# Performance work log

Measured on AMD Instinct MI355X. Metric: run time of the kernel, lower is better.

The kernel has to match this reference:

```python
import jax, jax.numpy as jnp
import numpy as np

NUM_EMBEDDINGS = 512
EMBEDDING_DIM = 64
COMMITMENT_COST = 0.25
DECAY = 0.99
EPSILON = 1e-05


def setup_inputs() -> dict:
    key = jax.random.key(0)
    k1, k2, k3 = jax.random.split(key, 3)
    inputs = jax.random.normal(k1, (32, 64, 64, EMBEDDING_DIM), dtype=jnp.float32)
    emb_w = jax.random.normal(k2, (NUM_EMBEDDINGS, EMBEDDING_DIM), dtype=jnp.float32)
    ema_cluster_size = jnp.ones((NUM_EMBEDDINGS,), dtype=jnp.float32)
    ema_w = jax.random.normal(k3, (NUM_EMBEDDINGS, EMBEDDING_DIM), dtype=jnp.float32)
    return {"inputs": inputs, "emb_w": emb_w,
            "ema_cluster_size": ema_cluster_size, "ema_w": ema_w}


def reference(inputs, emb_w, ema_cluster_size, ema_w):
    """VQ-VAE EMA quantizer forward (training=True path).

    inputs:           [B, H, W, D]  NHWC latents
    emb_w:            [K, D]        codebook (pre-update)
    ema_cluster_size: [K]           EMA cluster-size buffer
    ema_w:            [K, D]        EMA weight buffer
    """
    B, H, W, D = inputs.shape
    K = emb_w.shape[0]
    flat = inputs.reshape(-1, D)                                  # [N, D]

    distances = (jnp.sum(flat * flat, axis=1, keepdims=True)
                 - 2.0 * flat @ emb_w.T
                 + jnp.sum(emb_w * emb_w, axis=1))
    encoding_indices = jnp.argmin(distances, axis=1)              # [N]
    encodings = jax.nn.one_hot(encoding_indices, K, dtype=flat.dtype)  # [N, K]

    # --- EMA codebook update (buffer math; no gradient flows here) ---
    counts = jax.lax.stop_gradient(jnp.sum(encodings, axis=0))    # [K]
    cs = ema_cluster_size * DECAY + (1.0 - DECAY) * counts
    n = jnp.sum(cs)
    cs = (cs + EPSILON) / (n + K * EPSILON) * n                   # Laplace smoothing
    dw = jax.ops.segment_sum(jax.lax.stop_gradient(flat),
                             encoding_indices, num_segments=K)    # [K, D]
    new_ema_w = ema_w * DECAY + (1.0 - DECAY) * dw
    new_emb = new_ema_w / cs[:, None]                             # updated codebook

    # Quantize with the updated codebook (gather)
    quantized = new_emb[encoding_indices].reshape(B, H, W, D)

    # Commitment loss (quantized is detached)
    e_latent_loss = jnp.mean((jax.lax.stop_gradient(quantized) - inputs) ** 2)
    loss = COMMITMENT_COST * e_latent_loss

    # Straight-through estimator
    quantized_st = inputs + jax.lax.stop_gradient(quantized - inputs)

    avg_probs = jnp.mean(encodings, axis=0)
    perplexity = jnp.exp(-jnp.sum(avg_probs * jnp.log(avg_probs + 1e-10)))

    # NHWC -> NCHW as in the original return
    return loss, jnp.transpose(quantized_st, (0, 3, 1, 2)), perplexity, encodings
```

## Files before the change

kernel.cpp:

```cpp
#include <hip/hip_runtime.h>

#define DIM 64
#define K_CODES 512
#define N_VEC 131072
#define CREP 16
#define DREP 64
#define Q_OFF 1
#define PERP_OFF 8388609
#define ENC_OFF 8388610

using bfrag = __attribute__((ext_vector_type(8))) short;
using ffrag = __attribute__((ext_vector_type(4))) float;

__device__ __forceinline__ void split3(float x, short& h0, short& h1, short& h2)
{
    unsigned u0 = __float_as_uint(x);
    h0 = (short)(u0 >> 16);
    float r = x - __uint_as_float(u0 & 0xFFFF0000u);
    unsigned u1 = __float_as_uint(r);
    h1 = (short)(u1 >> 16);
    float r2 = r - __uint_as_float(u1 & 0xFFFF0000u);
    h2 = (short)(__float_as_uint(r2) >> 16);
}

__global__ __launch_bounds__(256) void epack_ee_kernel(
    const float* __restrict__ emb_w,
    bfrag* __restrict__ epack,
    float* __restrict__ ee,
    float* __restrict__ crep,
    float* __restrict__ lossac)
{
    __shared__ float part[2][16][8];
    const int tl = threadIdx.x;
    const int t = blockIdx.x * 256 + tl;
    const int lane = t & 63;
    const int db = (t >> 6) & 1;
    const int ctl = tl >> 7;
    const int ct = t >> 7;
    const int r16 = lane & 15, quad = lane >> 4;
    const int c  = ct * 16 + r16;
    const int d0 = db * 32 + quad * 8;
    const float* src = emb_w + (size_t)c * DIM + d0;

    crep[t] = 0.f;
    crep[4096 + t] = 0.f;
    if (t == 0) lossac[0] = 0.f;

    bfrag f0, f1, f2;
    float ssum = 0.f;
#pragma unroll
    for (int j = 0; j < 8; ++j) {
        const float x = src[j];
        ssum = fmaf(x, x, ssum);
        short a, b, cc;
        split3(x, a, b, cc);
        f0[j] = a; f1[j] = b; f2[j] = cc;
    }
    const int base = (ct * 2 + db) * 3;
    epack[(base + 0) * 64 + lane] = f0;
    epack[(base + 1) * 64 + lane] = f1;
    epack[(base + 2) * 64 + lane] = f2;

    part[ctl][r16][db * 4 + quad] = ssum;
    __syncthreads();
    if (tl < 32) {
        const int cl = tl >> 4, r = tl & 15;
        float s = 0.f;
#pragma unroll
        for (int i = 0; i < 8; ++i) s += part[cl][r][i];
        ee[(blockIdx.x * 2 + cl) * 16 + r] = s;
    }
}

__global__ __launch_bounds__(256, 4) void argmin_mfma_kernel(
    const float* __restrict__ inputs,
    const bfrag* __restrict__ epack,
    const float* __restrict__ eeg,
    int* __restrict__ idx,
    float* __restrict__ counts_rep)
{
    const int t = threadIdx.x;
    const int lane = t & 63;
    const int r16 = lane & 15;
    const int quad = lane >> 4;
    const size_t v0 = (size_t)blockIdx.x * 128 + (t >> 6) * 32;

    bfrag xf[2][2][3];
#pragma unroll
    for (int rt = 0; rt < 2; ++rt)
#pragma unroll
        for (int db = 0; db < 2; ++db) {
            const float* src = inputs + (v0 + rt * 16 + r16) * DIM + db * 32 + quad * 8;
            const float4 va = *reinterpret_cast<const float4*>(src);
            const float4 vb = *reinterpret_cast<const float4*>(src + 4);
            float vals[8] = {va.x, va.y, va.z, va.w, vb.x, vb.y, vb.z, vb.w};
            bfrag f0, f1, f2;
#pragma unroll
            for (int j = 0; j < 8; ++j) {
                short a, b, c;
                split3(vals[j], a, b, c);
                f0[j] = a; f1[j] = b; f2[j] = c;
            }
            xf[rt][db][0] = f0; xf[rt][db][1] = f1; xf[rt][db][2] = f2;
        }

    float best[2][4];
    int bestk[2][4];
#pragma unroll
    for (int a = 0; a < 2; ++a)
#pragma unroll
        for (int b = 0; b < 4; ++b) { best[a][b] = 3.4e38f; bestk[a][b] = 0; }

    constexpr int PI[6] = {0, 0, 1, 0, 2, 1};
    constexpr int PJ[6] = {0, 1, 0, 2, 0, 1};

    for (int ct = 0; ct < 32; ++ct) {
        bfrag e[2][3];
#pragma unroll
        for (int db = 0; db < 2; ++db)
#pragma unroll
            for (int s = 0; s < 3; ++s)
                e[db][s] = epack[((ct * 2 + db) * 3 + s) * 64 + lane];
        const float eel = eeg[ct * 16 + r16];

        ffrag acc[2];
        acc[0] = (ffrag){0.f, 0.f, 0.f, 0.f};
        acc[1] = (ffrag){0.f, 0.f, 0.f, 0.f};
#pragma unroll
        for (int db = 0; db < 2; ++db)
#pragma unroll
            for (int p = 0; p < 6; ++p) {
                acc[0] = __builtin_amdgcn_mfma_f32_16x16x32_bf16(
                    xf[0][db][PI[p]], e[db][PJ[p]], acc[0], 0, 0, 0);
                acc[1] = __builtin_amdgcn_mfma_f32_16x16x32_bf16(
                    xf[1][db][PI[p]], e[db][PJ[p]], acc[1], 0, 0, 0);
            }

        const int kc = ct * 16 + r16;
#pragma unroll
        for (int rt = 0; rt < 2; ++rt)
#pragma unroll
            for (int rg = 0; rg < 4; ++rg) {
                const float dist = fmaf(-2.f, acc[rt][rg], eel);
                if (dist < best[rt][rg]) { best[rt][rg] = dist; bestk[rt][rg] = kc; }
            }
    }

#pragma unroll
    for (int rt = 0; rt < 2; ++rt)
#pragma unroll
        for (int rg = 0; rg < 4; ++rg) {
            float b = best[rt][rg];
            int k = bestk[rt][rg];
#pragma unroll
            for (int m = 1; m < 16; m <<= 1) {
                const float ob = __shfl_xor(b, m, 64);
                const int ok = __shfl_xor(k, m, 64);
                if (ob < b || (ob == b && ok < k)) { b = ob; k = ok; }
            }
            bestk[rt][rg] = k;
        }

    if (r16 == 0) {
        float* crep = counts_rep + (blockIdx.x & (CREP - 1)) * K_CODES;
#pragma unroll
        for (int rt = 0; rt < 2; ++rt)
#pragma unroll
            for (int rg = 0; rg < 4; ++rg) {
                const int v = rt * 16 + quad * 4 + rg;
                const int k = bestk[rt][rg];
                idx[v0 + v] = k;
                atomicAdd(&crep[k], 1.0f);
            }
    }
}

__global__ __launch_bounds__(256) void enc_write_kernel(
    const int* __restrict__ idx,
    float* __restrict__ enc,
    float* __restrict__ dwrep)
{
    const size_t nf4 = 16777215;
    float4* body = reinterpret_cast<float4*>(enc + 2);
    const size_t stride = (size_t)gridDim.x * 256;

    for (size_t g = (size_t)blockIdx.x * 256 + threadIdx.x; g < nf4; g += stride) {
        const size_t e0 = 4 * g + 2;
        const int r0 = (int)(e0 >> 9);
        const int r1 = (int)((e0 + 3) >> 9);
        const int i0 = idx[r0];
        const int i1 = (r1 != r0) ? idx[r1] : i0;
        float4 v;
        v.x = ((int)(e0 & 511) == i0) ? 1.f : 0.f;
        v.y = ((int)((e0 + 1) & 511) == (((e0 + 1) >> 9) == (size_t)r0 ? i0 : i1)) ? 1.f : 0.f;
        v.z = ((int)((e0 + 2) & 511) == (((e0 + 2) >> 9) == (size_t)r0 ? i0 : i1)) ? 1.f : 0.f;
        v.w = ((int)((e0 + 3) & 511) == (((e0 + 3) >> 9) == (size_t)r0 ? i0 : i1)) ? 1.f : 0.f;
        body[g] = v;
    }

    float4* dw4 = reinterpret_cast<float4*>(dwrep);
    const size_t ndw4 = (size_t)DREP * K_CODES * DIM / 4;
    const float4 z = make_float4(0.f, 0.f, 0.f, 0.f);
    for (size_t i = (size_t)blockIdx.x * 256 + threadIdx.x; i < ndw4; i += stride)
        dw4[i] = z;

    if (blockIdx.x == 0 && threadIdx.x == 0) {
        const int k0 = idx[0];
        enc[0] = (k0 == 0) ? 1.f : 0.f;
        enc[1] = (k0 == 1) ? 1.f : 0.f;
        const int kL = idx[N_VEC - 1];
        enc[67108862] = (kL == 510) ? 1.f : 0.f;
        enc[67108863] = (kL == 511) ? 1.f : 0.f;
    }
}

__global__ __launch_bounds__(256) void dw_scatter_kernel(
    const float* __restrict__ inputs,
    const int* __restrict__ idx,
    float* __restrict__ dwrep)
{
    __shared__ int sIdx[256];
    const int t = threadIdx.x;
    const size_t vbase = (size_t)blockIdx.x * 256;
    sIdx[t] = idx[vbase + t];
    __syncthreads();
    const int w = t >> 6, lane = t & 63;
    const int v0 = w * 64;
#pragma unroll 4
    for (int j = 0; j < 64; ++j) {
        const int v = v0 + j;
        const int k = sIdx[v];
        const float xv = inputs[(vbase + v) * DIM + lane];
        atomicAdd(&dwrep[((size_t)(v & (DREP - 1)) << 15) + (k << 6) + lane], xv);
    }
}

__global__ __launch_bounds__(512) void emaA_kernel(
    const float* __restrict__ counts_rep,
    const float* __restrict__ ema_cs,
    float* __restrict__ csbuf,
    float* __restrict__ perp_out)
{
    __shared__ float red[K_CODES];
    const int k = threadIdx.x;
    float cnt = 0.f;
#pragma unroll
    for (int r = 0; r < CREP; ++r) cnt += counts_rep[r * K_CODES + k];
    float cs = ema_cs[k] * 0.99f + 0.01f * cnt;

    red[k] = cs;
    __syncthreads();
    for (int s = K_CODES / 2; s > 0; s >>= 1) {
        if (k < s) red[k] += red[k + s];
        __syncthreads();
    }
    const float n = red[0];
    __syncthreads();

    csbuf[k] = (cs + 1e-5f) / (n + (float)K_CODES * 1e-5f) * n;

    const float p = cnt * (1.0f / (float)N_VEC);
    red[k] = p * logf(p + 1e-10f);
    __syncthreads();
    for (int s = K_CODES / 2; s > 0; s >>= 1) {
        if (k < s) red[k] += red[k + s];
        __syncthreads();
    }
    if (k == 0) perp_out[0] = expf(-red[0]);
}

__global__ __launch_bounds__(256) void emaB_kernel(
    const float* __restrict__ dwrep,
    const float* __restrict__ ema_w,
    const float* __restrict__ csbuf,
    float* __restrict__ new_emb)
{
    const int t = blockIdx.x * 256 + threadIdx.x;
    const int k = t >> 6;
    float dwv = 0.f;
#pragma unroll
    for (int r = 0; r < DREP; ++r) dwv += dwrep[((size_t)r << 15) + t];
    const float v = ema_w[t] * 0.99f + 0.01f * dwv;
    new_emb[t] = v / csbuf[k];
}

__global__ __launch_bounds__(256) void quantize_kernel(
    const float* __restrict__ inputs,
    const int* __restrict__ idx,
    const float* __restrict__ new_emb,
    float* __restrict__ out_q,
    float* __restrict__ loss_accum)
{
    __shared__ int sIdx[64];
    __shared__ float tile[DIM][65];
    __shared__ float wsum[4];

    const int bh = blockIdx.x;
    const int b = bh >> 6, h = bh & 63;
    const int t = threadIdx.x;

    if (t < 64) sIdx[t] = idx[bh * 64 + t];
    __syncthreads();

    const float* inRow = inputs + (size_t)bh * 64 * DIM;
    const int d = t & 63;
    const int wg = t >> 6;
    float lsum = 0.f;
#pragma unroll
    for (int p = 0; p < 16; ++p) {
        const int w = wg * 16 + p;
        const float xv = inRow[w * DIM + d];
        const float qv = new_emb[sIdx[w] * DIM + d];
        const float diff = qv - xv;
        tile[d][w] = xv + diff;
        lsum = fmaf(diff, diff, lsum);
    }
    __syncthreads();

    const int w2 = t & 63;
    const int dg = t >> 6;
#pragma unroll
    for (int p = 0; p < 16; ++p) {
        const int d2 = dg * 16 + p;
        out_q[(((size_t)b * DIM + d2) * 64 + h) * 64 + w2] = tile[d2][w2];
    }

    for (int off = 32; off > 0; off >>= 1) lsum += __shfl_down(lsum, off);
    if ((t & 63) == 0) wsum[t >> 6] = lsum;
    __syncthreads();
    if (t == 0) atomicAdd(loss_accum, (wsum[0] + wsum[1]) + (wsum[2] + wsum[3]));
}

__global__ void finalize_kernel(const float* __restrict__ loss_accum,
                                float* __restrict__ out_loss)
{
    out_loss[0] = 0.25f * (loss_accum[0] / 8388608.0f);
}

extern "C" void kernel_launch(void* const* d_in, const int* in_sizes, int n_in,
                              void* d_out, int out_size, void* d_ws, size_t ws_size,
                              hipStream_t stream)
{
    const float* inputs = (const float*)d_in[0];
    const float* emb_w  = (const float*)d_in[1];
    const float* ema_cs = (const float*)d_in[2];
    const float* ema_w  = (const float*)d_in[3];
    float* out = (float*)d_out;
    float* ws  = (float*)d_ws;

    int*   idxbuf  = (int*)ws;
    float* crep    = ws + 131072;
    float* lossac  = ws + 139264;
    float* csbuf   = ws + 139265;
    float* eebuf   = ws + 139777;
    float* nemb    = ws + 140289;
    bfrag* epack   = (bfrag*)(ws + 173060);

    float* dwrep = out + 16;

    epack_ee_kernel<<<16, 256, 0, stream>>>(emb_w, epack, eebuf, crep, lossac);

    argmin_mfma_kernel<<<N_VEC / 128, 256, 0, stream>>>(
        inputs, epack, eebuf, idxbuf, crep);

    enc_write_kernel<<<2048, 256, 0, stream>>>(idxbuf, out + ENC_OFF, dwrep);

    dw_scatter_kernel<<<N_VEC / 256, 256, 0, stream>>>(inputs, idxbuf, dwrep);

    emaA_kernel<<<1, K_CODES, 0, stream>>>(crep, ema_cs, csbuf, out + PERP_OFF);
    emaB_kernel<<<K_CODES * DIM / 256, 256, 0, stream>>>(dwrep, ema_w, csbuf, nemb);

    quantize_kernel<<<32 * 64, 256, 0, stream>>>(
        inputs, idxbuf, nemb, out + Q_OFF, lossac);

    finalize_kernel<<<1, 1, 0, stream>>>(lossac, out);
}
```

Before: 216.7 us.

## Widen argmin tiles, fold dw zeroing into argmin, merge scatter with one-hot write

The argmin kernel now handles 256 vectors per block (four row tiles per wave instead of two), so each codebook fragment loaded is reused across more MFMAs. To fit the extra registers, launch bounds drop from 4 to 2 blocks per CU. The zeroing of the replicated dw buffer moves into the argmin kernel, each block clearing 1024 float4s. The dw scatter and one-hot encoding write are merged into a single launch with block-range dispatch, so the atomic scatter overlaps the bandwidth-bound encoding store and one launch is removed. The cost is lower occupancy in argmin and fewer grid-stride blocks writing the encodings.

```diff
diff --git a/kernel.cpp b/kernel.cpp
--- a/kernel.cpp
+++ b/kernel.cpp
@@ -8,6 +8,9 @@
 #define Q_OFF 1
 #define PERP_OFF 8388609
 #define ENC_OFF 8388610
+
+#define DW_BLOCKS 512
+#define ENC_BLOCKS 1280
 
 using bfrag = __attribute__((ext_vector_type(8))) short;
 using ffrag = __attribute__((ext_vector_type(4))) float;
@@ -72,22 +75,30 @@
     }
 }
 
-__global__ __launch_bounds__(256, 4) void argmin_mfma_kernel(
+__global__ __launch_bounds__(256, 2) void argmin_mfma_kernel(
     const float* __restrict__ inputs,
     const bfrag* __restrict__ epack,
     const float* __restrict__ eeg,
     int* __restrict__ idx,
-    float* __restrict__ counts_rep)
+    float* __restrict__ counts_rep,
+    float* __restrict__ dwrep)
 {
     const int t = threadIdx.x;
     const int lane = t & 63;
     const int r16 = lane & 15;
     const int quad = lane >> 4;
-    const size_t v0 = (size_t)blockIdx.x * 128 + (t >> 6) * 32;
-
-    bfrag xf[2][2][3];
-#pragma unroll
-    for (int rt = 0; rt < 2; ++rt)
+    const size_t v0 = (size_t)blockIdx.x * 256 + (t >> 6) * 64;
+
+    {
+        float4* z4 = reinterpret_cast<float4*>(dwrep) + (size_t)blockIdx.x * 1024;
+        const float4 z = make_float4(0.f, 0.f, 0.f, 0.f);
+#pragma unroll
+        for (int i = 0; i < 4; ++i) z4[i * 256 + t] = z;
+    }
+
+    bfrag xf[4][2][3];
+#pragma unroll
+    for (int rt = 0; rt < 4; ++rt)
 #pragma unroll
         for (int db = 0; db < 2; ++db) {
             const float* src = inputs + (v0 + rt * 16 + r16) * DIM + db * 32 + quad * 8;
@@ -104,16 +115,17 @@
             xf[rt][db][0] = f0; xf[rt][db][1] = f1; xf[rt][db][2] = f2;
         }
 
-    float best[2][4];
-    int bestk[2][4];
-#pragma unroll
-    for (int a = 0; a < 2; ++a)
+    float best[4][4];
+    int bestk[4][4];
+#pragma unroll
+    for (int a = 0; a < 4; ++a)
 #pragma unroll
         for (int b = 0; b < 4; ++b) { best[a][b] = 3.4e38f; bestk[a][b] = 0; }
 
     constexpr int PI[6] = {0, 0, 1, 0, 2, 1};
     constexpr int PJ[6] = {0, 1, 0, 2, 0, 1};
 
+#pragma unroll 2
     for (int ct = 0; ct < 32; ++ct) {
         bfrag e[2][3];
 #pragma unroll
@@ -123,22 +135,22 @@
                 e[db][s] = epack[((ct * 2 + db) * 3 + s) * 64 + lane];
         const float eel = eeg[ct * 16 + r16];
 
-        ffrag acc[2];
-        acc[0] = (ffrag){0.f, 0.f, 0.f, 0.f};
-        acc[1] = (ffrag){0.f, 0.f, 0.f, 0.f};
+        ffrag acc[4];
+#pragma unroll
+        for (int rt = 0; rt < 4; ++rt) acc[rt] = (ffrag){0.f, 0.f, 0.f, 0.f};
+
 #pragma unroll
         for (int db = 0; db < 2; ++db)
 #pragma unroll
-            for (int p = 0; p < 6; ++p) {
-                acc[0] = __builtin_amdgcn_mfma_f32_16x16x32_bf16(
-                    xf[0][db][PI[p]], e[db][PJ[p]], acc[0], 0, 0, 0);
-                acc[1] = __builtin_amdgcn_mfma_f32_16x16x32_bf16(
-                    xf[1][db][PI[p]], e[db][PJ[p]], acc[1], 0, 0, 0);
-            }
+            for (int p = 0; p < 6; ++p)
+#pragma unroll
+                for (int rt = 0; rt < 4; ++rt)
+                    acc[rt] = __builtin_amdgcn_mfma_f32_16x16x32_bf16(
+                        xf[rt][db][PI[p]], e[db][PJ[p]], acc[rt], 0, 0, 0);
 
         const int kc = ct * 16 + r16;
 #pragma unroll
-        for (int rt = 0; rt < 2; ++rt)
+        for (int rt = 0; rt < 4; ++rt)
 #pragma unroll
             for (int rg = 0; rg < 4; ++rg) {
                 const float dist = fmaf(-2.f, acc[rt][rg], eel);
@@ -147,7 +159,7 @@
     }
 
 #pragma unroll
-    for (int rt = 0; rt < 2; ++rt)
+    for (int rt = 0; rt < 4; ++rt)
 #pragma unroll
         for (int rg = 0; rg < 4; ++rg) {
             float b = best[rt][rg];
@@ -164,7 +176,7 @@
     if (r16 == 0) {
         float* crep = counts_rep + (blockIdx.x & (CREP - 1)) * K_CODES;
 #pragma unroll
-        for (int rt = 0; rt < 2; ++rt)
+        for (int rt = 0; rt < 4; ++rt)
 #pragma unroll
             for (int rg = 0; rg < 4; ++rg) {
                 const int v = rt * 16 + quad * 4 + rg;
@@ -175,63 +187,57 @@
     }
 }
 
-__global__ __launch_bounds__(256) void enc_write_kernel(
+__global__ __launch_bounds__(256) void encdw_kernel(
+    const float* __restrict__ inputs,
     const int* __restrict__ idx,
     float* __restrict__ enc,
     float* __restrict__ dwrep)
 {
-    const size_t nf4 = 16777215;
-    float4* body = reinterpret_cast<float4*>(enc + 2);
-    const size_t stride = (size_t)gridDim.x * 256;
-
-    for (size_t g = (size_t)blockIdx.x * 256 + threadIdx.x; g < nf4; g += stride) {
-        const size_t e0 = 4 * g + 2;
-        const int r0 = (int)(e0 >> 9);
-        const int r1 = (int)((e0 + 3) >> 9);
-        const int i0 = idx[r0];
-        const int i1 = (r1 != r0) ? idx[r1] : i0;
-        float4 v;
-        v.x = ((int)(e0 & 511) == i0) ? 1.f : 0.f;
-        v.y = ((int)((e0 + 1) & 511) == (((e0 + 1) >> 9) == (size_t)r0 ? i0 : i1)) ? 1.f : 0.f;
-        v.z = ((int)((e0 + 2) & 511) == (((e0 + 2) >> 9) == (size_t)r0 ? i0 : i1)) ? 1.f : 0.f;
-        v.w = ((int)((e0 + 3) & 511) == (((e0 + 3) >> 9) == (size_t)r0 ? i0 : i1)) ? 1.f : 0.f;
-        body[g] = v;
-    }
-
-    float4* dw4 = reinterpret_cast<float4*>(dwrep);
-    const size_t ndw4 = (size_t)DREP * K_CODES * DIM / 4;
-    const float4 z = make_float4(0.f, 0.f, 0.f, 0.f);
-    for (size_t i = (size_t)blockIdx.x * 256 + threadIdx.x; i < ndw4; i += stride)
-        dw4[i] = z;
-
-    if (blockIdx.x == 0 && threadIdx.x == 0) {
-        const int k0 = idx[0];
-        enc[0] = (k0 == 0) ? 1.f : 0.f;
-        enc[1] = (k0 == 1) ? 1.f : 0.f;
-        const int kL = idx[N_VEC - 1];
-        enc[67108862] = (kL == 510) ? 1.f : 0.f;
-        enc[67108863] = (kL == 511) ? 1.f : 0.f;
-    }
-}
-
-__global__ __launch_bounds__(256) void dw_scatter_kernel(
-    const float* __restrict__ inputs,
-    const int* __restrict__ idx,
-    float* __restrict__ dwrep)
-{
-    __shared__ int sIdx[256];
+    const int bid = blockIdx.x;
     const int t = threadIdx.x;
-    const size_t vbase = (size_t)blockIdx.x * 256;
-    sIdx[t] = idx[vbase + t];
-    __syncthreads();
-    const int w = t >> 6, lane = t & 63;
-    const int v0 = w * 64;
+
+    if (bid < DW_BLOCKS) {
+        __shared__ int sIdx[256];
+        const size_t vbase = (size_t)bid * 256;
+        sIdx[t] = idx[vbase + t];
+        __syncthreads();
+        const int w = t >> 6, lane = t & 63;
+        const int v0 = w * 64;
 #pragma unroll 4
-    for (int j = 0; j < 64; ++j) {
-        const int v = v0 + j;
-        const int k = sIdx[v];
-        const float xv = inputs[(vbase + v) * DIM + lane];
-        atomicAdd(&dwrep[((size_t)(v & (DREP - 1)) << 15) + (k << 6) + lane], xv);
+        for (int j = 0; j < 64; ++j) {
+            const int v = v0 + j;
+            const int k = sIdx[v];
+            const float xv = inputs[(vbase + v) * DIM + lane];
+            atomicAdd(&dwrep[((size_t)(v & (DREP - 1)) << 15) + (k << 6) + lane], xv);
+        }
+    } else {
+        const int eb = bid - DW_BLOCKS;
+        const size_t nf4 = 16777215;
+        float4* body = reinterpret_cast<float4*>(enc + 2);
+        const size_t stride = (size_t)ENC_BLOCKS * 256;
+
+        for (size_t g = (size_t)eb * 256 + t; g < nf4; g += stride) {
+            const size_t e0 = 4 * g + 2;
+            const int r0 = (int)(e0 >> 9);
+            const int r1 = (int)((e0 + 3) >> 9);
+            const int i0 = idx[r0];
+            const int i1 = (r1 != r0) ? idx[r1] : i0;
+            float4 v;
+            v.x = ((int)(e0 & 511) == i0) ? 1.f : 0.f;
+            v.y = ((int)((e0 + 1) & 511) == (((e0 + 1) >> 9) == (size_t)r0 ? i0 : i1)) ? 1.f : 0.f;
+            v.z = ((int)((e0 + 2) & 511) == (((e0 + 2) >> 9) == (size_t)r0 ? i0 : i1)) ? 1.f : 0.f;
+            v.w = ((int)((e0 + 3) & 511) == (((e0 + 3) >> 9) == (size_t)r0 ? i0 : i1)) ? 1.f : 0.f;
+            body[g] = v;
+        }
+
+        if (eb == 0 && t == 0) {
+            const int k0 = idx[0];
+            enc[0] = (k0 == 0) ? 1.f : 0.f;
+            enc[1] = (k0 == 1) ? 1.f : 0.f;
+            const int kL = idx[N_VEC - 1];
+            enc[67108862] = (kL == 510) ? 1.f : 0.f;
+            enc[67108863] = (kL == 511) ? 1.f : 0.f;
+        }
     }
 }
 
@@ -360,12 +366,11 @@
 
     epack_ee_kernel<<<16, 256, 0, stream>>>(emb_w, epack, eebuf, crep, lossac);
 
-    argmin_mfma_kernel<<<N_VEC / 128, 256, 0, stream>>>(
-        inputs, epack, eebuf, idxbuf, crep);
-
-    enc_write_kernel<<<2048, 256, 0, stream>>>(idxbuf, out + ENC_OFF, dwrep);
-
-    dw_scatter_kernel<<<N_VEC / 256, 256, 0, stream>>>(inputs, idxbuf, dwrep);
+    argmin_mfma_kernel<<<N_VEC / 256, 256, 0, stream>>>(
+        inputs, epack, eebuf, idxbuf, crep, dwrep);
+
+    encdw_kernel<<<DW_BLOCKS + ENC_BLOCKS, 256, 0, stream>>>(
+        inputs, idxbuf, out + ENC_OFF, dwrep);
 
     emaA_kernel<<<1, K_CODES, 0, stream>>>(crep, ema_cs, csbuf, out + PERP_OFF);
     emaB_kernel<<<K_CODES * DIM / 256, 256, 0, stream>>>(dwrep, ema_w, csbuf, nemb);
```

Result: faster. 184.3 us (-14.9%).

## Fuse one-hot write with dw scatter and move dw zeroing into argmin

Applied to the files above, without the earlier changes.

Zeroing of the dw replica buffer moves into the argmin kernel, where each block clears a 512-float4 slice. The encodings write and the dw atomic scatter are merged into one kernel whose blocks are split by role, so the scatter atomics overlap with the large one-hot store stream and one launch is removed. The argmin codebook loop also gets an unroll-2 hint and simplified epack addressing. Partitioning by block index risks load imbalance between the two roles, and the enc-block count is now fixed.

```diff
diff --git a/kernel.cpp b/kernel.cpp
--- a/kernel.cpp
+++ b/kernel.cpp
@@ -8,6 +8,10 @@
 #define Q_OFF 1
 #define PERP_OFF 8388609
 #define ENC_OFF 8388610
+
+#define DW_BLOCKS 512
+#define ENC_BLOCKS 1280
+#define QZ_BLOCKS 2048
 
 using bfrag = __attribute__((ext_vector_type(8))) short;
 using ffrag = __attribute__((ext_vector_type(4))) float;
@@ -77,13 +81,21 @@
     const bfrag* __restrict__ epack,
     const float* __restrict__ eeg,
     int* __restrict__ idx,
-    float* __restrict__ counts_rep)
+    float* __restrict__ counts_rep,
+    float* __restrict__ dwrep)
 {
     const int t = threadIdx.x;
     const int lane = t & 63;
     const int r16 = lane & 15;
     const int quad = lane >> 4;
     const size_t v0 = (size_t)blockIdx.x * 128 + (t >> 6) * 32;
+
+    {
+        float4* z4 = reinterpret_cast<float4*>(dwrep) + (size_t)blockIdx.x * 512;
+        const float4 z = make_float4(0.f, 0.f, 0.f, 0.f);
+#pragma unroll
+        for (int i = 0; i < 2; ++i) z4[i * 256 + t] = z;
+    }
 
     bfrag xf[2][2][3];
 #pragma unroll
@@ -114,13 +126,15 @@
     constexpr int PI[6] = {0, 0, 1, 0, 2, 1};
     constexpr int PJ[6] = {0, 1, 0, 2, 0, 1};
 
+#pragma unroll 2
     for (int ct = 0; ct < 32; ++ct) {
+        const bfrag* ep = epack + (size_t)ct * 384 + lane;
         bfrag e[2][3];
 #pragma unroll
         for (int db = 0; db < 2; ++db)
 #pragma unroll
             for (int s = 0; s < 3; ++s)
-                e[db][s] = epack[((ct * 2 + db) * 3 + s) * 64 + lane];
+                e[db][s] = ep[(db * 3 + s) * 64];
         const float eel = eeg[ct * 16 + r16];
 
         ffrag acc[2];
@@ -175,63 +189,57 @@
     }
 }
 
-__global__ __launch_bounds__(256) void enc_write_kernel(
+__global__ __launch_bounds__(256) void encdw_kernel(
+    const float* __restrict__ inputs,
     const int* __restrict__ idx,
     float* __restrict__ enc,
     float* __restrict__ dwrep)
 {
-    const size_t nf4 = 16777215;
-    float4* body = reinterpret_cast<float4*>(enc + 2);
-    const size_t stride = (size_t)gridDim.x * 256;
-
-    for (size_t g = (size_t)blockIdx.x * 256 + threadIdx.x; g < nf4; g += stride) {
-        const size_t e0 = 4 * g + 2;
-        const int r0 = (int)(e0 >> 9);
-        const int r1 = (int)((e0 + 3) >> 9);
-        const int i0 = idx[r0];
-        const int i1 = (r1 != r0) ? idx[r1] : i0;
-        float4 v;
-        v.x = ((int)(e0 & 511) == i0) ? 1.f : 0.f;
-        v.y = ((int)((e0 + 1) & 511) == (((e0 + 1) >> 9) == (size_t)r0 ? i0 : i1)) ? 1.f : 0.f;
-        v.z = ((int)((e0 + 2) & 511) == (((e0 + 2) >> 9) == (size_t)r0 ? i0 : i1)) ? 1.f : 0.f;
-        v.w = ((int)((e0 + 3) & 511) == (((e0 + 3) >> 9) == (size_t)r0 ? i0 : i1)) ? 1.f : 0.f;
-        body[g] = v;
-    }
-
-    float4* dw4 = reinterpret_cast<float4*>(dwrep);
-    const size_t ndw4 = (size_t)DREP * K_CODES * DIM / 4;
-    const float4 z = make_float4(0.f, 0.f, 0.f, 0.f);
-    for (size_t i = (size_t)blockIdx.x * 256 + threadIdx.x; i < ndw4; i += stride)
-        dw4[i] = z;
-
-    if (blockIdx.x == 0 && threadIdx.x == 0) {
-        const int k0 = idx[0];
-        enc[0] = (k0 == 0) ? 1.f : 0.f;
-        enc[1] = (k0 == 1) ? 1.f : 0.f;
-        const int kL = idx[N_VEC - 1];
-        enc[67108862] = (kL == 510) ? 1.f : 0.f;
-        enc[67108863] = (kL == 511) ? 1.f : 0.f;
-    }
-}
-
-__global__ __launch_bounds__(256) void dw_scatter_kernel(
-    const float* __restrict__ inputs,
-    const int* __restrict__ idx,
-    float* __restrict__ dwrep)
-{
-    __shared__ int sIdx[256];
+    const int bid = blockIdx.x;
     const int t = threadIdx.x;
-    const size_t vbase = (size_t)blockIdx.x * 256;
-    sIdx[t] = idx[vbase + t];
-    __syncthreads();
-    const int w = t >> 6, lane = t & 63;
-    const int v0 = w * 64;
+
+    if (bid < DW_BLOCKS) {
+        __shared__ int sIdx[256];
+        const size_t vbase = (size_t)bid * 256;
+        sIdx[t] = idx[vbase + t];
+        __syncthreads();
+        const int w = t >> 6, lane = t & 63;
+        const int v0 = w * 64;
 #pragma unroll 4
-    for (int j = 0; j < 64; ++j) {
-        const int v = v0 + j;
-        const int k = sIdx[v];
-        const float xv = inputs[(vbase + v) * DIM + lane];
-        atomicAdd(&dwrep[((size_t)(v & (DREP - 1)) << 15) + (k << 6) + lane], xv);
+        for (int j = 0; j < 64; ++j) {
+            const int v = v0 + j;
+            const int k = sIdx[v];
+            const float xv = inputs[(vbase + v) * DIM + lane];
+            atomicAdd(&dwrep[((size_t)(v & (DREP - 1)) << 15) + (k << 6) + lane], xv);
+        }
+    } else {
+        const int eb = bid - DW_BLOCKS;
+        const size_t nf4 = 16777215;
+        float4* body = reinterpret_cast<float4*>(enc + 2);
+        const size_t stride = (size_t)ENC_BLOCKS * 256;
+
+        for (size_t g = (size_t)eb * 256 + t; g < nf4; g += stride) {
+            const size_t e0 = 4 * g + 2;
+            const int r0 = (int)(e0 >> 9);
+            const int r1 = (int)((e0 + 3) >> 9);
+            const int i0 = idx[r0];
+            const int i1 = (r1 != r0) ? idx[r1] : i0;
+            float4 v;
+            v.x = ((int)(e0 & 511) == i0) ? 1.f : 0.f;
+            v.y = ((int)((e0 + 1) & 511) == (((e0 + 1) >> 9) == (size_t)r0 ? i0 : i1)) ? 1.f : 0.f;
+            v.z = ((int)((e0 + 2) & 511) == (((e0 + 2) >> 9) == (size_t)r0 ? i0 : i1)) ? 1.f : 0.f;
+            v.w = ((int)((e0 + 3) & 511) == (((e0 + 3) >> 9) == (size_t)r0 ? i0 : i1)) ? 1.f : 0.f;
+            body[g] = v;
+        }
+
+        if (eb == 0 && t == 0) {
+            const int k0 = idx[0];
+            enc[0] = (k0 == 0) ? 1.f : 0.f;
+            enc[1] = (k0 == 1) ? 1.f : 0.f;
+            const int kL = idx[N_VEC - 1];
+            enc[67108862] = (kL == 510) ? 1.f : 0.f;
+            enc[67108863] = (kL == 511) ? 1.f : 0.f;
+        }
     }
 }
 
@@ -361,16 +369,15 @@
     epack_ee_kernel<<<16, 256, 0, stream>>>(emb_w, epack, eebuf, crep, lossac);
 
     argmin_mfma_kernel<<<N_VEC / 128, 256, 0, stream>>>(
-        inputs, epack, eebuf, idxbuf, crep);
-
-    enc_write_kernel<<<2048, 256, 0, stream>>>(idxbuf, out + ENC_OFF, dwrep);
-
-    dw_scatter_kernel<<<N_VEC / 256, 256, 0, stream>>>(inputs, idxbuf, dwrep);
+        inputs, epack, eebuf, idxbuf, crep, dwrep);
+
+    encdw_kernel<<<DW_BLOCKS + ENC_BLOCKS, 256, 0, stream>>>(
+        inputs, idxbuf, out + ENC_OFF, dwrep);
 
     emaA_kernel<<<1, K_CODES, 0, stream>>>(crep, ema_cs, csbuf, out + PERP_OFF);
     emaB_kernel<<<K_CODES * DIM / 256, 256, 0, stream>>>(dwrep, ema_w, csbuf, nemb);
 
-    quantize_kernel<<<32 * 64, 256, 0, stream>>>(
+    quantize_kernel<<<QZ_BLOCKS, 256, 0, stream>>>(
         inputs, idxbuf, nemb, out + Q_OFF, lossac);
 
     finalize_kernel<<<1, 1, 0, stream>>>(lossac, out);
```

Result: faster. 181.8 us (median of 2 runs) (-16.1%).
